# Optimization experiments

Measured on AMD Instinct MI355X. Metric: run time of the kernel, lower is better.

The kernel has to match this reference:

```python
import jax, jax.numpy as jnp
import numpy as np

B, S, D = 4, 2048, 768
H = 12
HD = D // H  # 64


def setup_inputs() -> dict:
    key = jax.random.key(0)
    ks = jax.random.split(key, 9)
    scale = 0.02
    return {
        "hidden_states": jax.random.normal(ks[0], (B, S, D), dtype=jnp.float32),
        "Wq": jax.random.normal(ks[1], (D, D), dtype=jnp.float32) * scale,
        "bq": jnp.zeros((D,), dtype=jnp.float32),
        "Wk": jax.random.normal(ks[2], (D, D), dtype=jnp.float32) * scale,
        "bk": jnp.zeros((D,), dtype=jnp.float32),
        "Wv": jax.random.normal(ks[3], (D, D), dtype=jnp.float32) * scale,
        "bv": jnp.zeros((D,), dtype=jnp.float32),
        "Wo": jax.random.normal(ks[4], (D, D), dtype=jnp.float32) * scale,
        "bo": jnp.zeros((D,), dtype=jnp.float32),
    }


def reference(hidden_states, Wq, bq, Wk, bk, Wv, bv, Wo, bo):
    b, s, d = hidden_states.shape
    inv_sqrt_hd = 1.0 / jnp.sqrt(jnp.asarray(HD, dtype=hidden_states.dtype))

    def split_heads(x):  # [b, s, d] -> [b, h, s, hd]
        return x.reshape(b, s, H, HD).transpose(0, 2, 1, 3)

    q = split_heads(hidden_states @ Wq + bq)
    k = split_heads(hidden_states @ Wk + bk)
    v = split_heads(hidden_states @ Wv + bv)

    scores = jnp.einsum("bhqd,bhkd->bhqk", q, k) * inv_sqrt_hd
    probs = jax.nn.softmax(scores, axis=-1)
    ctx = jnp.einsum("bhqk,bhkd->bhqd", probs, v)  # [b, h, s, hd]
    ctx = ctx.transpose(0, 2, 1, 3).reshape(b, s, d)
    return ctx @ Wo + bo
```

## Files before the change

kernel.cpp:

```cpp
#include <hip/hip_runtime.h>

typedef unsigned short u16;
typedef __attribute__((ext_vector_type(4))) float f32x4;
typedef __attribute__((ext_vector_type(16))) float f32x16;
typedef __attribute__((ext_vector_type(8))) __bf16 bf16x8;
typedef __attribute__((ext_vector_type(8))) unsigned short u16x8;
typedef __attribute__((ext_vector_type(2))) unsigned u32x2;

#define L2E 1.44269504088896340736f

#if __has_builtin(__builtin_amdgcn_exp2f)
#define EXP2(x) __builtin_amdgcn_exp2f(x)
#else
#define EXP2(x) exp2f(x)
#endif

__device__ __forceinline__ u16 f2bf(float f) {
  unsigned u = __float_as_uint(f);
  u += 0x7fffu + ((u >> 16) & 1u);
  return (u16)(u >> 16);
}

__device__ __forceinline__ unsigned pk2(float a, float b) {
  __bf16 x = (__bf16)a, y = (__bf16)b;
  unsigned short ux = __builtin_bit_cast(unsigned short, x);
  unsigned short uy = __builtin_bit_cast(unsigned short, y);
  return (unsigned)ux | ((unsigned)uy << 16);
}

__device__ __forceinline__ bf16x8 as_bf(uint4 v) { return __builtin_bit_cast(bf16x8, v); }

__device__ __forceinline__ u32x2 plswap(unsigned a, unsigned b) {
#if __has_builtin(__builtin_amdgcn_permlane32_swap)
  auto t = __builtin_amdgcn_permlane32_swap(a, b, false, false);
  return __builtin_bit_cast(u32x2, t);
#else
  unsigned pa = (unsigned)__shfl_xor((int)a, 32, 64);
  unsigned pb = (unsigned)__shfl_xor((int)b, 32, 64);
  const bool hi = (threadIdx.x & 32) != 0;
  u32x2 r;
  r.x = hi ? pb : a;
  r.y = hi ? b : pa;
  return r;
#endif
}

__device__ __forceinline__ void gl2lds16(const void* g, void* l) {
  __builtin_amdgcn_global_load_lds((const __attribute__((address_space(1))) void*)g,
                                   (__attribute__((address_space(3))) void*)l, 16, 0, 0);
}

__global__ void cvt_hs(const float* __restrict__ in, u16* __restrict__ out, int n4) {
  int i = blockIdx.x * 256 + threadIdx.x;
  if (i < n4) {
    float4 v = ((const float4*)in)[i];
    ushort4 o;
    o.x = f2bf(v.x); o.y = f2bf(v.y); o.z = f2bf(v.z); o.w = f2bf(v.w);
    ((ushort4*)out)[i] = o;
  }
}

__global__ void cvt_w(const float* __restrict__ Wq, const float* __restrict__ Wk,
                      const float* __restrict__ Wv, const float* __restrict__ Wo,
                      u16* __restrict__ wt, u16* __restrict__ wot) {
  __shared__ float ts[32][33];
  const int w = blockIdx.z;
  const float* src = (w == 0) ? Wq : (w == 1) ? Wk : (w == 2) ? Wv : Wo;
  u16* dst = (w < 3) ? (wt + (size_t)w * 768 * 768) : wot;
  const float scale = (w == 0) ? 0.125f * L2E : 1.0f;
  const int n0 = blockIdx.x * 32, k0 = blockIdx.y * 32;
  const int tx = threadIdx.x, ty = threadIdx.y;
#pragma unroll
  for (int j = 0; j < 4; ++j)
    ts[ty + 8 * j][tx] = src[(size_t)(k0 + ty + 8 * j) * 768 + n0 + tx];
  __syncthreads();
#pragma unroll
  for (int j = 0; j < 4; ++j)
    dst[(size_t)(n0 + ty + 8 * j) * 768 + k0 + tx] = f2bf(ts[tx][ty + 8 * j] * scale);
}

template <int MODE>
__global__ void gemm_bt(const u16* __restrict__ A, const u16* __restrict__ Bt,
                        const float* __restrict__ b0, const float* __restrict__ b1,
                        const float* __restrict__ b2, void* __restrict__ Cout,
                        int M, int N, int K, int nbx) {
  __shared__ u16 As[3][128 * 32];
  __shared__ u16 Bs[3][128 * 32];
  const int tid = threadIdx.x;
  const int lane = tid & 63, wid = tid >> 6;
  const int wr = wid >> 1, wc = wid & 1;
  const int l15 = lane & 15, lg = lane >> 4;

  const int nwg = gridDim.x;
  const int cpx = nwg >> 3;
  const int p = blockIdx.x;
  const int wg = (p & 7) * cpx + (p >> 3);
  const int mblk = (wg / nbx) * 128, nblk = (wg % nbx) * 128;

  f32x4 acc[4][4] = {};

  const int srow = lane >> 2;
  const int skc = (lane & 3) * 8;
  const int rr0 = 32 * wid, rr1 = 32 * wid + 16;

  const u16* ap0 = A + (size_t)(mblk + rr0 + srow) * K + skc;
  const u16* ap1 = A + (size_t)(mblk + rr1 + srow) * K + skc;
  const u16* bp0 = Bt + (size_t)(nblk + rr0 + srow) * K + skc;
  const u16* bp1 = Bt + (size_t)(nblk + rr1 + srow) * K + skc;

#define GSTAGE(buf)                             \
  {                                             \
    gl2lds16(ap0, &As[buf][rr0 * 32]);          \
    gl2lds16(ap1, &As[buf][rr1 * 32]);          \
    gl2lds16(bp0, &Bs[buf][rr0 * 32]);          \
    gl2lds16(bp1, &Bs[buf][rr1 * 32]);          \
    ap0 += 32; ap1 += 32; bp0 += 32; bp1 += 32; \
  }

  const int nt = K >> 5;
  GSTAGE(0);
  GSTAGE(1);
  asm volatile("s_waitcnt vmcnt(4)" ::: "memory");
  __builtin_amdgcn_s_barrier();
  __builtin_amdgcn_sched_barrier(0);

  int cur = 0, stg = 2;
#pragma unroll 1
  for (int t = 0; t < nt; ++t) {
    const bool more = (t + 2 < nt);
    if (more) GSTAGE(stg);
    bf16x8 af[4], bfr[4];
#pragma unroll
    for (int i = 0; i < 4; ++i) {
      af[i] = as_bf(*(const uint4*)&As[cur][(64 * wr + 16 * i + l15) * 32 + 8 * lg]);
      bfr[i] = as_bf(*(const uint4*)&Bs[cur][(64 * wc + 16 * i + l15) * 32 + 8 * lg]);
    }
    __builtin_amdgcn_s_setprio(1);
#pragma unroll
    for (int mi = 0; mi < 4; ++mi)
#pragma unroll
      for (int ni = 0; ni < 4; ++ni)
        acc[mi][ni] = __builtin_amdgcn_mfma_f32_16x16x32_bf16(af[mi], bfr[ni], acc[mi][ni], 0, 0, 0);
    __builtin_amdgcn_s_setprio(0);
    if (more)
      asm volatile("s_waitcnt vmcnt(4)" ::: "memory");
    else
      asm volatile("s_waitcnt vmcnt(0)" ::: "memory");
    __builtin_amdgcn_s_barrier();
    __builtin_amdgcn_sched_barrier(0);
    cur = (cur == 2) ? 0 : cur + 1;
    stg = (stg == 2) ? 0 : stg + 1;
  }
#undef GSTAGE

#pragma unroll
  for (int ni = 0; ni < 4; ++ni) {
    const int col = nblk + 64 * wc + 16 * ni + l15;
    float bias;
    if (MODE == 0) {
      if (col < 768) bias = b0[col] * (0.125f * L2E);
      else if (col < 1536) bias = b1[col - 768];
      else bias = b2[col - 1536];
    } else {
      bias = b0[col];
    }
#pragma unroll
    for (int mi = 0; mi < 4; ++mi) {
#pragma unroll
      for (int r = 0; r < 4; ++r) {
        const int row = mblk + 64 * wr + 16 * mi + 4 * lg + r;
        const float v = acc[mi][ni][r] + bias;
        if (MODE == 0)
          ((u16*)Cout)[(size_t)row * N + col] = f2bf(v);
        else
          ((float*)Cout)[(size_t)row * N + col] = v;
      }
    }
  }
}

__global__ void tr_v(const u16* __restrict__ qkv, u16* __restrict__ vt) {
  __shared__ u16 t[64][72];
  const int tid = threadIdx.x;
  const int st = blockIdx.x, h = blockIdx.y, b = blockIdx.z;
  const u16* vsrc = qkv + (size_t)b * 2048 * 2304 + 1536 + h * 64;
  const int s0 = st * 64;
#pragma unroll
  for (int i = 0; i < 2; ++i) {
    const int seg = tid + 256 * i;
    const int row = seg >> 3, slot = seg & 7;
    *(uint4*)&t[row][slot * 8] = *(const uint4*)(vsrc + (size_t)(s0 + row) * 2304 + slot * 8);
  }
  __syncthreads();
  u16* dst = vt + (size_t)(b * 12 + h) * 64 * 2048;
#pragma unroll
  for (int i = 0; i < 2; ++i) {
    const int seg = tid + 256 * i;
    const int hd = seg >> 3, j0 = (seg & 7) * 8;
    u16x8 o;
#pragma unroll
    for (int j = 0; j < 8; ++j) o[j] = t[j0 + j][hd];
    *(u16x8*)(dst + (size_t)hd * 2048 + s0 + j0) = o;
  }
}

__global__ void __launch_bounds__(256, 3)
attn_fwd(const u16* __restrict__ qkv, const u16* __restrict__ vt, u16* __restrict__ ctx) {
  __shared__ u16 Ks[2][64 * 64];
  __shared__ u16 Vs[2][64 * 64];

  const int tid = threadIdx.x;
  const int lane = tid & 63, wid = tid >> 6;
  const int l31 = lane & 31, H = lane >> 5;
  const int r7 = l31 & 7;

  const int p = blockIdx.x;
  const int l = 96 * (p & 7) + (p >> 3);
  const int qb = l & 15;
  const int hb = l >> 4;
  const int h = hb % 12;
  const int b = hb / 12;

  const u16* qbase = qkv + (size_t)b * 2048 * 2304 + h * 64;
  const u16* kbase = qbase + 768;
  const u16* vbase = vt + (size_t)(b * 12 + h) * 64 * 2048;

  const int srow = tid >> 3;
  const int sx = (tid & 7) ^ (srow & 7);
  const int dseg = (tid & ~63) * 8;

  const u16* kp0 = kbase + (size_t)srow * 2304 + 8 * sx;
  const u16* kp1 = kbase + (size_t)(srow + 32) * 2304 + 8 * sx;
  const u16* vp0 = vbase + (size_t)srow * 2048 + 8 * sx;
  const u16* vp1 = vbase + (size_t)(srow + 32) * 2048 + 8 * sx;

  unsigned koff[2][4];
#pragma unroll
  for (int t32 = 0; t32 < 2; ++t32)
#pragma unroll
    for (int ks = 0; ks < 4; ++ks)
      koff[t32][ks] = (32 * t32 + l31) * 64 + 8 * ((2 * ks + H) ^ r7);

  const int q0 = qb * 128 + wid * 32;
  bf16x8 qf[4];
#pragma unroll
  for (int ks = 0; ks < 4; ++ks)
    qf[ks] = as_bf(*(const uint4*)(qbase + (size_t)(q0 + l31) * 2304 + 16 * ks + 8 * H));

  float lsum = 0.f;
  f32x16 o[2] = {};

#define STAGE(buf)                              \
  {                                             \
    gl2lds16(kp0, &Ks[buf][dseg]);              \
    gl2lds16(kp1, &Ks[buf][dseg + 2048]);       \
    gl2lds16(vp0, &Vs[buf][dseg]);              \
    gl2lds16(vp1, &Vs[buf][dseg + 2048]);       \
    kp0 += 64 * 2304; kp1 += 64 * 2304;         \
    vp0 += 64; vp1 += 64;                       \
  }

#define PHASE(CUR)                                                                        \
  {                                                                                       \
    f32x16 st[2] = {};                                                                    \
    __builtin_amdgcn_s_setprio(1);                                                        \
    _Pragma("unroll") for (int k32 = 0; k32 < 2; ++k32)                                   \
        _Pragma("unroll") for (int ks = 0; ks < 4; ++ks) {                                \
      bf16x8 kf = as_bf(*(const uint4*)&Ks[CUR][koff[k32][ks]]);                          \
      st[k32] = __builtin_amdgcn_mfma_f32_32x32x16_bf16(kf, qf[ks], st[k32], 0, 0, 0);    \
    }                                                                                     \
    __builtin_amdgcn_s_setprio(0);                                                        \
                                                         \
    float s0 = 0.f, s1 = 0.f, s2 = 0.f, s3 = 0.f;                                         \
    _Pragma("unroll") for (int k32 = 0; k32 < 2; ++k32)                                   \
        _Pragma("unroll") for (int r = 0; r < 16; r += 4) {                               \
      float e0 = EXP2(st[k32][r + 0]);                                                    \
      float e1 = EXP2(st[k32][r + 1]);                                                    \
      float e2 = EXP2(st[k32][r + 2]);                                                    \
      float e3 = EXP2(st[k32][r + 3]);                                                    \
      st[k32][r + 0] = e0; st[k32][r + 1] = e1;                                           \
      st[k32][r + 2] = e2; st[k32][r + 3] = e3;                                           \
      s0 += e0; s1 += e1; s2 += e2; s3 += e3;                                             \
    }                                                                                     \
    lsum += (s0 + s1) + (s2 + s3);                                                        \
                                              \
    bf16x8 pf[4];                                                                         \
    _Pragma("unroll") for (int ks = 0; ks < 4; ++ks) {                                    \
      const int k32 = ks >> 1, rb = 8 * (ks & 1);                                         \
      unsigned a0 = pk2(st[k32][rb + 0], st[k32][rb + 1]);                                \
      unsigned a1 = pk2(st[k32][rb + 2], st[k32][rb + 3]);                                \
      unsigned a2 = pk2(st[k32][rb + 4], st[k32][rb + 5]);                                \
      unsigned a3 = pk2(st[k32][rb + 6], st[k32][rb + 7]);                                \
      u32x2 s02 = plswap(a0, a2);                                                         \
      u32x2 s13 = plswap(a1, a3);                                                         \
      uint4 w;                                                                            \
      w.x = s02.x; w.y = s13.x; w.z = s02.y; w.w = s13.y;                                 \
      pf[ks] = as_bf(w);                                                                  \
    }                                                                                     \
                                                                      \
    __builtin_amdgcn_s_setprio(1);                                                        \
    _Pragma("unroll") for (int d32 = 0; d32 < 2; ++d32)                                   \
        _Pragma("unroll") for (int ks = 0; ks < 4; ++ks) {                                \
      bf16x8 vf = as_bf(*(const uint4*)&Vs[CUR][koff[d32][ks]]);                          \
      o[d32] = __builtin_amdgcn_mfma_f32_32x32x16_bf16(vf, pf[ks], o[d32], 0, 0, 0);      \
    }                                                                                     \
    __builtin_amdgcn_s_setprio(0);                                                        \
    __syncthreads();                                                                      \
  }

  STAGE(0);
  __syncthreads();

#pragma unroll 1
  for (int cc = 0; cc < 16; ++cc) {
    const int c2 = 2 * cc;
    STAGE(1);
    PHASE(0);
    if (c2 + 2 < 32) STAGE(0);
    PHASE(1);
  }
#undef PHASE
#undef STAGE

  const float ls = lsum + __shfl_xor(lsum, 32, 64);
  const float inv = 1.0f / ls;
  const size_t rowoff = ((size_t)b * 2048 + q0 + l31) * 768 + h * 64;
#pragma unroll
  for (int d32 = 0; d32 < 2; ++d32)
#pragma unroll
    for (int g = 0; g < 4; ++g) {
      uint2 w;
      w.x = pk2(o[d32][4 * g + 0] * inv, o[d32][4 * g + 1] * inv);
      w.y = pk2(o[d32][4 * g + 2] * inv, o[d32][4 * g + 3] * inv);
      *(uint2*)&ctx[rowoff + 32 * d32 + 8 * g + 4 * H] = w;
    }
}

extern "C" void kernel_launch(void* const* d_in, const int* in_sizes, int n_in,
                              void* d_out, int out_size, void* d_ws, size_t ws_size,
                              hipStream_t stream) {
  const float* hs = (const float*)d_in[0];
  const float* Wq = (const float*)d_in[1];
  const float* bq = (const float*)d_in[2];
  const float* Wk = (const float*)d_in[3];
  const float* bk = (const float*)d_in[4];
  const float* Wv = (const float*)d_in[5];
  const float* bv = (const float*)d_in[6];
  const float* Wo = (const float*)d_in[7];
  const float* bo = (const float*)d_in[8];

  char* ws = (char*)d_ws;
  u16* hsb = (u16*)ws;
  u16* wt  = (u16*)(ws + 12582912);
  u16* wot = (u16*)(ws + 16121856);
  u16* qkv = (u16*)(ws + 17301504);
  u16* vt  = (u16*)(ws + 55050240);
  u16* ctx = (u16*)(ws + 67633152);

  cvt_hs<<<dim3(6144), dim3(256), 0, stream>>>(hs, hsb, 8192 * 768 / 4);
  cvt_w<<<dim3(24, 24, 4), dim3(32, 8), 0, stream>>>(Wq, Wk, Wv, Wo, wt, wot);
  gemm_bt<0><<<dim3(18 * 64), dim3(256), 0, stream>>>(hsb, wt, bq, bk, bv, (void*)qkv,
                                                      8192, 2304, 768, 18);
  tr_v<<<dim3(32, 12, 4), dim3(256), 0, stream>>>(qkv, vt);
  attn_fwd<<<dim3(768), dim3(256), 0, stream>>>(qkv, vt, ctx);
  gemm_bt<1><<<dim3(6 * 64), dim3(256), 0, stream>>>(ctx, wot, bo, bo, bo, d_out,
                                                     8192, 768, 768, 6);
}
```

Before: 154.5 us.

## Fuse V transpose into QKV GEMM epilogue and swizzle GEMM LDS layout

Removes the separate tr_v kernel by having the QKV projection GEMM also write each V element directly into the transposed vt buffer from its epilogue. It also XOR-swizzles the 16-byte chunk placement in the GEMM's LDS tiles to reduce bank conflicts on the fragment reads. The price is an extra scattered 2-byte store per V element with a stride-2048 pattern, which may coalesce poorly and slow the epilogue. It saves one kernel launch and a full read and write pass over V.

```diff
diff --git a/kernel.cpp b/kernel.cpp
--- a/kernel.cpp
+++ b/kernel.cpp
@@ -83,13 +83,14 @@
 __global__ void gemm_bt(const u16* __restrict__ A, const u16* __restrict__ Bt,
                         const float* __restrict__ b0, const float* __restrict__ b1,
                         const float* __restrict__ b2, void* __restrict__ Cout,
-                        int M, int N, int K, int nbx) {
+                        u16* __restrict__ vt_out, int M, int N, int K, int nbx) {
   __shared__ u16 As[3][128 * 32];
   __shared__ u16 Bs[3][128 * 32];
   const int tid = threadIdx.x;
   const int lane = tid & 63, wid = tid >> 6;
   const int wr = wid >> 1, wc = wid & 1;
   const int l15 = lane & 15, lg = lane >> 4;
+  const int lgx = lg ^ ((l15 >> 1) & 3);
 
   const int nwg = gridDim.x;
   const int cpx = nwg >> 3;
@@ -100,7 +101,7 @@
   f32x4 acc[4][4] = {};
 
   const int srow = lane >> 2;
-  const int skc = (lane & 3) * 8;
+  const int skc = ((lane & 3) ^ ((srow >> 1) & 3)) * 8;
   const int rr0 = 32 * wid, rr1 = 32 * wid + 16;
 
   const u16* ap0 = A + (size_t)(mblk + rr0 + srow) * K + skc;
@@ -132,8 +133,8 @@
     bf16x8 af[4], bfr[4];
 #pragma unroll
     for (int i = 0; i < 4; ++i) {
-      af[i] = as_bf(*(const uint4*)&As[cur][(64 * wr + 16 * i + l15) * 32 + 8 * lg]);
-      bfr[i] = as_bf(*(const uint4*)&Bs[cur][(64 * wc + 16 * i + l15) * 32 + 8 * lg]);
+      af[i] = as_bf(*(const uint4*)&As[cur][(64 * wr + 16 * i + l15) * 32 + 8 * lgx]);
+      bfr[i] = as_bf(*(const uint4*)&Bs[cur][(64 * wc + 16 * i + l15) * 32 + 8 * lgx]);
     }
     __builtin_amdgcn_s_setprio(1);
 #pragma unroll
@@ -157,10 +158,15 @@
   for (int ni = 0; ni < 4; ++ni) {
     const int col = nblk + 64 * wc + 16 * ni + l15;
     float bias;
+    u16* vdst = nullptr;
     if (MODE == 0) {
       if (col < 768) bias = b0[col] * (0.125f * L2E);
       else if (col < 1536) bias = b1[col - 768];
       else bias = b2[col - 1536];
+      if (col >= 1536) {
+        const int vcol = col - 1536;
+        vdst = vt_out + ((size_t)((mblk >> 11) * 12 + (vcol >> 6)) * 64 + (vcol & 63)) * 2048;
+      }
     } else {
       bias = b0[col];
     }
@@ -170,37 +176,15 @@
       for (int r = 0; r < 4; ++r) {
         const int row = mblk + 64 * wr + 16 * mi + 4 * lg + r;
         const float v = acc[mi][ni][r] + bias;
-        if (MODE == 0)
-          ((u16*)Cout)[(size_t)row * N + col] = f2bf(v);
-        else
+        if (MODE == 0) {
+          const u16 bv = f2bf(v);
+          ((u16*)Cout)[(size_t)row * N + col] = bv;
+          if (vdst) vdst[row & 2047] = bv;
+        } else {
           ((float*)Cout)[(size_t)row * N + col] = v;
+        }
       }
     }
-  }
-}
-
-__global__ void tr_v(const u16* __restrict__ qkv, u16* __restrict__ vt) {
-  __shared__ u16 t[64][72];
-  const int tid = threadIdx.x;
-  const int st = blockIdx.x, h = blockIdx.y, b = blockIdx.z;
-  const u16* vsrc = qkv + (size_t)b * 2048 * 2304 + 1536 + h * 64;
-  const int s0 = st * 64;
-#pragma unroll
-  for (int i = 0; i < 2; ++i) {
-    const int seg = tid + 256 * i;
-    const int row = seg >> 3, slot = seg & 7;
-    *(uint4*)&t[row][slot * 8] = *(const uint4*)(vsrc + (size_t)(s0 + row) * 2304 + slot * 8);
-  }
-  __syncthreads();
-  u16* dst = vt + (size_t)(b * 12 + h) * 64 * 2048;
-#pragma unroll
-  for (int i = 0; i < 2; ++i) {
-    const int seg = tid + 256 * i;
-    const int hd = seg >> 3, j0 = (seg & 7) * 8;
-    u16x8 o;
-#pragma unroll
-    for (int j = 0; j < 8; ++j) o[j] = t[j0 + j][hd];
-    *(u16x8*)(dst + (size_t)hd * 2048 + s0 + j0) = o;
   }
 }
 
@@ -360,9 +344,8 @@
   cvt_hs<<<dim3(6144), dim3(256), 0, stream>>>(hs, hsb, 8192 * 768 / 4);
   cvt_w<<<dim3(24, 24, 4), dim3(32, 8), 0, stream>>>(Wq, Wk, Wv, Wo, wt, wot);
   gemm_bt<0><<<dim3(18 * 64), dim3(256), 0, stream>>>(hsb, wt, bq, bk, bv, (void*)qkv,
-                                                      8192, 2304, 768, 18);
-  tr_v<<<dim3(32, 12, 4), dim3(256), 0, stream>>>(qkv, vt);
+                                                      vt, 8192, 2304, 768, 18);
   attn_fwd<<<dim3(768), dim3(256), 0, stream>>>(qkv, vt, ctx);
   gemm_bt<1><<<dim3(6 * 64), dim3(256), 0, stream>>>(ctx, wot, bo, bo, bo, d_out,
-                                                     8192, 768, 768, 6);
-}
+                                                     nullptr, 8192, 768, 768, 6);
+}
```

Result: slower. 167.0 us (+8.1%).

## Merge input conversion kernels and XOR-swizzle GEMM LDS tiles

Applied to the files above, without the earlier changes.

Combines the hidden-state bf16 conversion and the weight transpose/convert into a single launch, saving one kernel launch and its tail. Separately, the GEMM now applies an XOR swizzle to the 16-byte chunk index on both the global-to-LDS staging and the fragment reads, to reduce LDS bank conflicts on the 32-element-wide rows. The merged kernel has a branch on block index, and the transpose blocks run after all conversion blocks.

```diff
diff --git a/kernel.cpp b/kernel.cpp
--- a/kernel.cpp
+++ b/kernel.cpp
@@ -50,26 +50,29 @@
                                    (__attribute__((address_space(3))) void*)l, 16, 0, 0);
 }
 
-__global__ void cvt_hs(const float* __restrict__ in, u16* __restrict__ out, int n4) {
-  int i = blockIdx.x * 256 + threadIdx.x;
-  if (i < n4) {
-    float4 v = ((const float4*)in)[i];
+__global__ void prep(const float* __restrict__ hs, const float* __restrict__ Wq,
+                     const float* __restrict__ Wk, const float* __restrict__ Wv,
+                     const float* __restrict__ Wo, u16* __restrict__ hsb,
+                     u16* __restrict__ wt, u16* __restrict__ wot) {
+  const int blk = blockIdx.x;
+  const int tid = threadIdx.x;
+  if (blk < 6144) {
+    const int i = blk * 256 + tid;
+    float4 v = ((const float4*)hs)[i];
     ushort4 o;
     o.x = f2bf(v.x); o.y = f2bf(v.y); o.z = f2bf(v.z); o.w = f2bf(v.w);
-    ((ushort4*)out)[i] = o;
-  }
-}
-
-__global__ void cvt_w(const float* __restrict__ Wq, const float* __restrict__ Wk,
-                      const float* __restrict__ Wv, const float* __restrict__ Wo,
-                      u16* __restrict__ wt, u16* __restrict__ wot) {
+    ((ushort4*)hsb)[i] = o;
+    return;
+  }
   __shared__ float ts[32][33];
-  const int w = blockIdx.z;
+  const int idx = blk - 6144;
+  const int w = idx / 576;
+  const int rem = idx % 576;
+  const int n0 = (rem % 24) * 32, k0 = (rem / 24) * 32;
   const float* src = (w == 0) ? Wq : (w == 1) ? Wk : (w == 2) ? Wv : Wo;
   u16* dst = (w < 3) ? (wt + (size_t)w * 768 * 768) : wot;
   const float scale = (w == 0) ? 0.125f * L2E : 1.0f;
-  const int n0 = blockIdx.x * 32, k0 = blockIdx.y * 32;
-  const int tx = threadIdx.x, ty = threadIdx.y;
+  const int tx = tid & 31, ty = tid >> 5;
 #pragma unroll
   for (int j = 0; j < 4; ++j)
     ts[ty + 8 * j][tx] = src[(size_t)(k0 + ty + 8 * j) * 768 + n0 + tx];
@@ -90,6 +93,7 @@
   const int lane = tid & 63, wid = tid >> 6;
   const int wr = wid >> 1, wc = wid & 1;
   const int l15 = lane & 15, lg = lane >> 4;
+  const int lgx = lg ^ ((l15 >> 1) & 3);
 
   const int nwg = gridDim.x;
   const int cpx = nwg >> 3;
@@ -100,7 +104,7 @@
   f32x4 acc[4][4] = {};
 
   const int srow = lane >> 2;
-  const int skc = (lane & 3) * 8;
+  const int skc = ((lane & 3) ^ ((srow >> 1) & 3)) * 8;
   const int rr0 = 32 * wid, rr1 = 32 * wid + 16;
 
   const u16* ap0 = A + (size_t)(mblk + rr0 + srow) * K + skc;
@@ -132,8 +136,8 @@
     bf16x8 af[4], bfr[4];
 #pragma unroll
     for (int i = 0; i < 4; ++i) {
-      af[i] = as_bf(*(const uint4*)&As[cur][(64 * wr + 16 * i + l15) * 32 + 8 * lg]);
-      bfr[i] = as_bf(*(const uint4*)&Bs[cur][(64 * wc + 16 * i + l15) * 32 + 8 * lg]);
+      af[i] = as_bf(*(const uint4*)&As[cur][(64 * wr + 16 * i + l15) * 32 + 8 * lgx]);
+      bfr[i] = as_bf(*(const uint4*)&Bs[cur][(64 * wc + 16 * i + l15) * 32 + 8 * lgx]);
     }
     __builtin_amdgcn_s_setprio(1);
 #pragma unroll
@@ -357,8 +361,7 @@
   u16* vt  = (u16*)(ws + 55050240);
   u16* ctx = (u16*)(ws + 67633152);
 
-  cvt_hs<<<dim3(6144), dim3(256), 0, stream>>>(hs, hsb, 8192 * 768 / 4);
-  cvt_w<<<dim3(24, 24, 4), dim3(32, 8), 0, stream>>>(Wq, Wk, Wv, Wo, wt, wot);
+  prep<<<dim3(8448), dim3(256), 0, stream>>>(hs, Wq, Wk, Wv, Wo, hsb, wt, wot);
   gemm_bt<0><<<dim3(18 * 64), dim3(256), 0, stream>>>(hsb, wt, bq, bk, bv, (void*)qkv,
                                                       8192, 2304, 768, 18);
   tr_v<<<dim3(32, 12, 4), dim3(256), 0, stream>>>(qkv, vt);
```

Result: faster. 151.3 us (-2.0%).
